# Kernel optimization log

Measured on AMD Instinct MI355X. Metric: run time of the kernel, lower is better.

The kernel has to match this reference:

```python
import jax, jax.numpy as jnp
import numpy as np

GRID_SIZE = 16
SPLINE_ORDER = 4
GRID_LO, GRID_HI = -1.0, 1.0
NUM_GRID = 2 * SPLINE_ORDER + GRID_SIZE + 1  # 25 knots
NUM_COEFFS = GRID_SIZE + SPLINE_ORDER        # 20 basis functions
B, IN_F, OUT_F = 2048, 512, 512


def _make_grid():
    h = (GRID_HI - GRID_LO) / GRID_SIZE
    t1 = -SPLINE_ORDER * h + GRID_LO
    t2 = (GRID_SIZE + SPLINE_ORDER + 1) * h + GRID_LO
    return jnp.linspace(t1, t2, NUM_GRID)


def _bspline_basis(x, grid):
    # x: [..., in]; returns [..., in, NUM_COEFFS] via De Boor recursion
    xe = x[..., None]
    bases = ((xe >= grid[:-1]) & (xe < grid[1:])).astype(x.dtype)
    for k in range(1, SPLINE_ORDER + 1):
        left = (xe - grid[:-k - 1]) / (grid[k:-1] - grid[:-k - 1]) * bases[..., :-1]
        right = (grid[k + 1:] - xe) / (grid[k + 1:] - grid[1:-k]) * bases[..., 1:]
        bases = left + right
    return bases


def setup_inputs() -> dict:
    key = jax.random.key(0)
    ks = jax.random.split(key, 5)
    fan = np.sqrt(1.0 / IN_F)
    return {
        "x": jax.random.normal(ks[0], (B, IN_F), jnp.float32),
        "prelu_weight": jax.random.normal(ks[1], (OUT_F, IN_F), jnp.float32) * 0.25,
        "base_weight": jax.random.uniform(ks[2], (OUT_F, IN_F), jnp.float32, -fan, fan),
        "spline_weight": jax.random.uniform(ks[3], (OUT_F, IN_F), jnp.float32, -fan, fan),
        "spline_coeffs": jax.random.normal(ks[4], (OUT_F, IN_F, NUM_COEFFS), jnp.float32) * 0.1,
    }


def reference(x, prelu_weight, base_weight, spline_weight, spline_coeffs):
    grid = _make_grid()
    xc = jnp.clip(x, GRID_LO, GRID_HI)
    pos = jax.nn.relu(xc)
    neg = xc - pos
    # base path: sum_j base_w[i,j]*(prelu_w[i,j]*neg[b,j] + pos[b,j])
    # fused: never materialize the [out, B, in] prelu output
    base = neg @ (base_weight * prelu_weight).T + pos @ base_weight.T  # [B, out]
    basis = _bspline_basis(xc, grid)  # [B, in, K]
    # spline path: fold spline_weight into coeffs, single contraction over (j,k)
    eff_coeffs = spline_weight[:, :, None] * spline_coeffs  # [out, in, K]
    spline = jnp.einsum('bjk,ijk->bi', basis, eff_coeffs)   # [B, out]
    return base + spline
```

## Files before the change

### kernel.cpp

```cpp
#include <hip/hip_runtime.h>


typedef _Float16 half_t;
typedef __attribute__((ext_vector_type(8))) _Float16 half8;
typedef __attribute__((ext_vector_type(4))) float floatx4;

#define B_DIM   2048
#define J_DIM   512
#define O_DIM   512
#define SLOTS   22
#define K_TOT   (J_DIM * SLOTS)
#define MTILE   128
#define NTILE   128
#define BK      32
#define KSPLIT  11
#define KS_LEN  (K_TOT / KSPLIT)
#define KCH     (KS_LEN / BK)
#define ZERO_BLKS 64

__device__ __forceinline__ void bspline5(float xc, int& k0, float Nv[5]) {
    const float invS = 7.68f;
    float u = (xc + 1.5f) * invS;
    int m = (int)u;
    m = min(max(m, 3), 19);
    k0 = m - 4;
    Nv[0] = 1.f; Nv[1] = 0.f; Nv[2] = 0.f; Nv[3] = 0.f; Nv[4] = 0.f;
#pragma unroll
    for (int d = 1; d <= 4; ++d) {
        float nw[5];
        float inv_d = 1.0f / (float)d;
#pragma unroll
        for (int r = 0; r < 5; ++r) {
            if (r > d) { nw[r] = 0.f; continue; }
            float kk = (float)(m - d + r);
            float acc = 0.f;
            if (r >= 1) acc += (u - kk) * Nv[r - 1];
            if (r < d)  acc += (kk + (float)(d + 1) - u) * Nv[r];
            nw[r] = acc * inv_d;
        }
#pragma unroll
        for (int r = 0; r < 5; ++r) Nv[r] = nw[r];
    }
}

__global__ __launch_bounds__(256) void prep_all(const float* __restrict__ x,
                                                const float* __restrict__ pw,
                                                const float* __restrict__ bw,
                                                const float* __restrict__ sw,
                                                const float* __restrict__ sc,
                                                half_t* __restrict__ A,
                                                half_t* __restrict__ Ct,
                                                float* __restrict__ out) {
    __shared__ half_t rec[J_DIM * SLOTS];
    int bid = blockIdx.x;
    int t = threadIdx.x;

    if (bid < ZERO_BLKS) {
        float4* o = (float4*)out;
        int base = bid * 4096;
#pragma unroll
        for (int i = 0; i < 16; ++i)
            o[base + i * 256 + t] = make_float4(0.f, 0.f, 0.f, 0.f);
        return;
    }

    if (bid < ZERO_BLKS + O_DIM) {
        int i = bid - ZERO_BLKS;
#pragma unroll
        for (int jj = 0; jj < 2; ++jj) {
            int j = t + jj * 256;
            size_t ij = (size_t)i * J_DIM + j;
            float s = sw[ij], b = bw[ij], p = pw[ij];
            const float4* scp4 = (const float4*)(sc + ij * 20);
            half_t* r = rec + j * SLOTS;
#pragma unroll
            for (int v = 0; v < 5; ++v) {
                float4 c4 = scp4[v];
                r[v * 4 + 0] = (half_t)(s * c4.x);
                r[v * 4 + 1] = (half_t)(s * c4.y);
                r[v * 4 + 2] = (half_t)(s * c4.z);
                r[v * 4 + 3] = (half_t)(s * c4.w);
            }
            r[20] = (half_t)(b * p);
            r[21] = (half_t)b;
        }
        __syncthreads();
        const uint4* src = (const uint4*)rec;
        uint4* dst = (uint4*)(Ct + (size_t)i * K_TOT);
        for (int idx = t; idx < (J_DIM * SLOTS * 2) / 16; idx += 256) dst[idx] = src[idx];
        return;
    }

    int b = bid - ZERO_BLKS - O_DIM;
#pragma unroll
    for (int jj = 0; jj < 2; ++jj) {
        int j = t + jj * 256;
        float xv = x[(size_t)b * J_DIM + j];
        float xc = fminf(fmaxf(xv, -1.f), 1.f);
        float pos = fmaxf(xc, 0.f);
        float neg = xc - pos;
        int k0; float Nv[5];
        bspline5(xc, k0, Nv);
        half_t* r = rec + j * SLOTS;
#pragma unroll
        for (int k = 0; k < 20; ++k) r[k] = (half_t)0.f;
#pragma unroll
        for (int rr = 0; rr < 5; ++rr) {
            int k = k0 + rr;
            if (k >= 0) r[k] = (half_t)Nv[rr];
        }
        r[20] = (half_t)neg;
        r[21] = (half_t)pos;
    }
    __syncthreads();
    const uint4* src = (const uint4*)rec;
    uint4* dst = (uint4*)(A + (size_t)b * K_TOT);
    for (int i = t; i < (J_DIM * SLOTS * 2) / 16; i += 256) dst[i] = src[i];
}

__global__ __launch_bounds__(256, 4) void gemm_f16(const half_t* __restrict__ A,
                                                   const half_t* __restrict__ Bt,
                                                   float* __restrict__ out) {
    __shared__ half_t As[2][MTILE * BK];
    __shared__ half_t Bs[2][NTILE * BK];

    int m0 = blockIdx.x * MTILE;
    int n0 = blockIdx.y * NTILE;
    int ks = blockIdx.z * KS_LEN;

    int t = threadIdx.x;
    int w = t >> 6;
    int l = t & 63;
    int wm = w >> 1, wn = w & 1;

    floatx4 acc[4][4] = {};

    int lrow = l >> 2;
    int lkof = (((l & 3) ^ ((l >> 3) & 3)) * 8);

    const half_t* gA = A + (size_t)m0 * K_TOT + ks;
    const half_t* gB = Bt + (size_t)n0 * K_TOT + ks;

    int q = l >> 4;
    int fr = l & 15;
    int qs = (q ^ ((fr >> 1) & 3)) * 8;

#define ISSUE_LOADS(c, p)                                                     \
    {                                                                         \
        int kb = (c) * BK;                                                    \
        _Pragma("unroll")                                                     \
        for (int n = 0; n < 2; ++n) {                                         \
            int r = (w * 2 + n) * 16 + lrow;                                  \
            __builtin_amdgcn_global_load_lds(                                 \
                (const __attribute__((address_space(1))) unsigned int*)       \
                    (gA + (size_t)r * K_TOT + kb + lkof),                     \
                (__attribute__((address_space(3))) unsigned int*)             \
                    (&As[p][0] + (w * 2 + n) * 512),                          \
                16, 0, 0);                                                    \
            __builtin_amdgcn_global_load_lds(                                 \
                (const __attribute__((address_space(1))) unsigned int*)       \
                    (gB + (size_t)r * K_TOT + kb + lkof),                     \
                (__attribute__((address_space(3))) unsigned int*)             \
                    (&Bs[p][0] + (w * 2 + n) * 512),                          \
                16, 0, 0);                                                    \
        }                                                                     \
    }

    ISSUE_LOADS(0, 0)
    int p = 0;
    for (int c = 0; c < KCH; ++c) {
        __syncthreads();
        if (c + 1 < KCH) ISSUE_LOADS(c + 1, p ^ 1)

        half8 af[4], bf[4];
#pragma unroll
        for (int mt = 0; mt < 4; ++mt)
            af[mt] = *(const half8*)(&As[p][0] + (wm * 64 + mt * 16 + fr) * BK + qs);
#pragma unroll
        for (int nt = 0; nt < 4; ++nt)
            bf[nt] = *(const half8*)(&Bs[p][0] + (wn * 64 + nt * 16 + fr) * BK + qs);
#pragma unroll
        for (int mt = 0; mt < 4; ++mt)
#pragma unroll
            for (int nt = 0; nt < 4; ++nt)
                acc[mt][nt] = __builtin_amdgcn_mfma_f32_16x16x32_f16(
                    af[mt], bf[nt], acc[mt][nt], 0, 0, 0);
        p ^= 1;
    }
#undef ISSUE_LOADS

#pragma unroll
    for (int mt = 0; mt < 4; ++mt)
#pragma unroll
        for (int nt = 0; nt < 4; ++nt) {
            int rr = m0 + wm * 64 + mt * 16 + q * 4;
            int cc = n0 + wn * 64 + nt * 16 + fr;
#pragma unroll
            for (int r = 0; r < 4; ++r)
                atomicAdd(out + (size_t)(rr + r) * O_DIM + cc, acc[mt][nt][r]);
        }
}

__global__ __launch_bounds__(256) void kan_fallback(const float* __restrict__ x,
                                                    const float* __restrict__ pw,
                                                    const float* __restrict__ bw,
                                                    const float* __restrict__ sw,
                                                    const float* __restrict__ sc,
                                                    float* __restrict__ out) {
    __shared__ float s_neg[J_DIM], s_pos[J_DIM], s_bas[J_DIM][5];
    __shared__ int s_k0[J_DIM];
    int b = blockIdx.x;
    int t = threadIdx.x;
#pragma unroll
    for (int jj = 0; jj < 2; ++jj) {
        int j = t + jj * 256;
        float xv = x[(size_t)b * J_DIM + j];
        float xc = fminf(fmaxf(xv, -1.f), 1.f);
        float pos = fmaxf(xc, 0.f);
        s_pos[j] = pos;
        s_neg[j] = xc - pos;
        int k0; float Nv[5];
        bspline5(xc, k0, Nv);
        s_k0[j] = k0;
#pragma unroll
        for (int r = 0; r < 5; ++r) s_bas[j][r] = Nv[r];
    }
    __syncthreads();
    for (int i = t; i < O_DIM; i += 256) {
        float acc = 0.f;
        for (int j = 0; j < J_DIM; ++j) {
            size_t ij = (size_t)i * J_DIM + j;
            float bwv = bw[ij];
            acc += bwv * (pw[ij] * s_neg[j] + s_pos[j]);
            int k0 = s_k0[j];
            const float* cp = sc + ij * 20;
            float sp = 0.f;
#pragma unroll
            for (int r = 0; r < 5; ++r) {
                int k = k0 + r;
                if (k >= 0) sp += s_bas[j][r] * cp[k];
            }
            acc += sw[ij] * sp;
        }
        out[(size_t)b * O_DIM + i] = acc;
    }
}

extern "C" void kernel_launch(void* const* d_in, const int* in_sizes, int n_in,
                              void* d_out, int out_size, void* d_ws, size_t ws_size,
                              hipStream_t stream) {
    const float* x  = (const float*)d_in[0];
    const float* pw = (const float*)d_in[1];
    const float* bw = (const float*)d_in[2];
    const float* sw = (const float*)d_in[3];
    const float* sc = (const float*)d_in[4];
    float* out = (float*)d_out;

    const size_t ws_needed = (size_t)(B_DIM + O_DIM) * K_TOT * sizeof(half_t);
    if (ws_size < ws_needed) {
        kan_fallback<<<B_DIM, 256, 0, stream>>>(x, pw, bw, sw, sc, out);
        return;
    }

    half_t* A  = (half_t*)d_ws;
    half_t* Ct = A + (size_t)B_DIM * K_TOT;

    prep_all<<<ZERO_BLKS + O_DIM + B_DIM, 256, 0, stream>>>(x, pw, bw, sw, sc, A, Ct, out);
    dim3 g(B_DIM / MTILE, O_DIM / NTILE, KSPLIT);
    gemm_f16<<<g, 256, 0, stream>>>(A, Ct, out);
}
```

Baseline: 142.5 us.

## Rewrite KAN pipeline with 256x256 split-K GEMM, partial buffers and reduce kernel

The GEMM moves from 128x128x32 tiles with atomicAdd split-K to 256x256x64 tiles with 512 threads, 16-way split-K and a block-index swizzle. Each K-split writes a private partial buffer, and a separate reduce kernel sums the partials, which removes float atomics and the output zeroing. Prep is rewritten to vectorize packing of weights and activations. The cost is extra workspace, a third launch and the traffic of 16 full partial outputs. Loads are staged with explicit vmcnt waits and setprio phases.

```diff
diff --git a/kernel.cpp b/kernel.cpp
--- a/kernel.cpp
+++ b/kernel.cpp
@@ -10,13 +10,10 @@
 #define O_DIM   512
 #define SLOTS   22
 #define K_TOT   (J_DIM * SLOTS)
-#define MTILE   128
-#define NTILE   128
-#define BK      32
-#define KSPLIT  11
-#define KS_LEN  (K_TOT / KSPLIT)
-#define KCH     (KS_LEN / BK)
-#define ZERO_BLKS 64
+#define BM      256
+#define BN      256
+#define BK      64
+#define KSPLIT  16
 
 __device__ __forceinline__ void bspline5(float xc, int& k0, float Nv[5]) {
     const float invS = 7.68f;
@@ -43,162 +40,224 @@
     }
 }
 
-__global__ __launch_bounds__(256) void prep_all(const float* __restrict__ x,
-                                                const float* __restrict__ pw,
-                                                const float* __restrict__ bw,
-                                                const float* __restrict__ sw,
-                                                const float* __restrict__ sc,
-                                                half_t* __restrict__ A,
-                                                half_t* __restrict__ Ct,
-                                                float* __restrict__ out) {
-    __shared__ half_t rec[J_DIM * SLOTS];
+__device__ __forceinline__ unsigned packh2(float a, float b) {
+    half_t ha = (half_t)a, hb = (half_t)b;
+    unsigned short ua = __builtin_bit_cast(unsigned short, ha);
+    unsigned short ub = __builtin_bit_cast(unsigned short, hb);
+    return (unsigned)ua | ((unsigned)ub << 16);
+}
+
+__global__ __launch_bounds__(256) void prep2(const float* __restrict__ x,
+                                             const float* __restrict__ pw,
+                                             const float* __restrict__ bw,
+                                             const float* __restrict__ sw,
+                                             const float* __restrict__ sc,
+                                             half_t* __restrict__ A,
+                                             half_t* __restrict__ Ct) {
+    __shared__ half_t sbuf[2][128 * 88];
     int bid = blockIdx.x;
     int t = threadIdx.x;
-
-    if (bid < ZERO_BLKS) {
-        float4* o = (float4*)out;
-        int base = bid * 4096;
-#pragma unroll
-        for (int i = 0; i < 16; ++i)
-            o[base + i * 256 + t] = make_float4(0.f, 0.f, 0.f, 0.f);
+    int sub = t >> 7;
+    int jq  = t & 127;
+    int j0  = jq * 4;
+
+    if (bid < 256) {
+        int i = bid * 2 + sub;
+        size_t ij0 = (size_t)i * J_DIM + j0;
+        float4 s4 = *(const float4*)(sw + ij0);
+        float4 b4 = *(const float4*)(bw + ij0);
+        float4 p4 = *(const float4*)(pw + ij0);
+        const float4* sp4 = (const float4*)(sc + ij0 * 20);
+        unsigned u[44];
+#pragma unroll
+        for (int jj = 0; jj < 4; ++jj) {
+            float s = ((const float*)&s4)[jj];
+            float b = ((const float*)&b4)[jj];
+            float p = ((const float*)&p4)[jj];
+#pragma unroll
+            for (int v = 0; v < 5; ++v) {
+                float4 c4 = sp4[jj * 5 + v];
+                u[jj * 11 + v * 2 + 0] = packh2(s * c4.x, s * c4.y);
+                u[jj * 11 + v * 2 + 1] = packh2(s * c4.z, s * c4.w);
+            }
+            u[jj * 11 + 10] = packh2(b * p, b);
+        }
+        uint4* dst = (uint4*)(Ct + (size_t)i * K_TOT + (size_t)j0 * SLOTS);
+#pragma unroll
+        for (int v = 0; v < 11; ++v)
+            dst[v] = make_uint4(u[4 * v], u[4 * v + 1], u[4 * v + 2], u[4 * v + 3]);
         return;
     }
 
-    if (bid < ZERO_BLKS + O_DIM) {
-        int i = bid - ZERO_BLKS;
-#pragma unroll
-        for (int jj = 0; jj < 2; ++jj) {
-            int j = t + jj * 256;
-            size_t ij = (size_t)i * J_DIM + j;
-            float s = sw[ij], b = bw[ij], p = pw[ij];
-            const float4* scp4 = (const float4*)(sc + ij * 20);
-            half_t* r = rec + j * SLOTS;
-#pragma unroll
-            for (int v = 0; v < 5; ++v) {
-                float4 c4 = scp4[v];
-                r[v * 4 + 0] = (half_t)(s * c4.x);
-                r[v * 4 + 1] = (half_t)(s * c4.y);
-                r[v * 4 + 2] = (half_t)(s * c4.z);
-                r[v * 4 + 3] = (half_t)(s * c4.w);
-            }
-            r[20] = (half_t)(b * p);
-            r[21] = (half_t)b;
-        }
-        __syncthreads();
-        const uint4* src = (const uint4*)rec;
-        uint4* dst = (uint4*)(Ct + (size_t)i * K_TOT);
-        for (int idx = t; idx < (J_DIM * SLOTS * 2) / 16; idx += 256) dst[idx] = src[idx];
-        return;
-    }
-
-    int b = bid - ZERO_BLKS - O_DIM;
-#pragma unroll
-    for (int jj = 0; jj < 2; ++jj) {
-        int j = t + jj * 256;
-        float xv = x[(size_t)b * J_DIM + j];
+    int b0 = (bid - 256) * 2;
+    int b = b0 + sub;
+    float4 x4 = *(const float4*)(x + (size_t)b * J_DIM + j0);
+    half_t* reg = &sbuf[sub][jq * 88];
+
+    half8 z;
+#pragma unroll
+    for (int e = 0; e < 8; ++e) z[e] = (half_t)0.f;
+#pragma unroll
+    for (int v = 0; v < 11; ++v) *(half8*)(reg + v * 8) = z;
+
+#pragma unroll
+    for (int jj = 0; jj < 4; ++jj) {
+        float xv = ((const float*)&x4)[jj];
         float xc = fminf(fmaxf(xv, -1.f), 1.f);
         float pos = fmaxf(xc, 0.f);
         float neg = xc - pos;
         int k0; float Nv[5];
         bspline5(xc, k0, Nv);
-        half_t* r = rec + j * SLOTS;
-#pragma unroll
-        for (int k = 0; k < 20; ++k) r[k] = (half_t)0.f;
+        half_t* rb = reg + jj * SLOTS;
 #pragma unroll
         for (int rr = 0; rr < 5; ++rr) {
             int k = k0 + rr;
-            if (k >= 0) r[k] = (half_t)Nv[rr];
-        }
-        r[20] = (half_t)neg;
-        r[21] = (half_t)pos;
+            if (k >= 0) rb[k] = (half_t)Nv[rr];
+        }
+        *(unsigned*)(rb + 20) = packh2(neg, pos);
     }
     __syncthreads();
-    const uint4* src = (const uint4*)rec;
-    uint4* dst = (uint4*)(A + (size_t)b * K_TOT);
-    for (int i = t; i < (J_DIM * SLOTS * 2) / 16; i += 256) dst[i] = src[i];
-}
-
-__global__ __launch_bounds__(256, 4) void gemm_f16(const half_t* __restrict__ A,
-                                                   const half_t* __restrict__ Bt,
-                                                   float* __restrict__ out) {
-    __shared__ half_t As[2][MTILE * BK];
-    __shared__ half_t Bs[2][NTILE * BK];
-
-    int m0 = blockIdx.x * MTILE;
-    int n0 = blockIdx.y * NTILE;
-    int ks = blockIdx.z * KS_LEN;
+
+    const uint4* src = (const uint4*)&sbuf[0][0];
+    uint4* dst = (uint4*)(A + (size_t)b0 * K_TOT);
+#pragma unroll
+    for (int v = 0; v < 11; ++v) dst[v * 256 + t] = src[v * 256 + t];
+}
+
+__global__ __launch_bounds__(512, 2) void gemm16_f16(const half_t* __restrict__ A,
+                                                     const half_t* __restrict__ Bt,
+                                                     float* __restrict__ out) {
+    constexpr int KS_LEN = K_TOT / KSPLIT;
+    constexpr int NSTEP = KS_LEN / BK;
+
+    __shared__ half_t As[2][BM * BK];
+    __shared__ half_t Bs[2][BN * BK];
+
+    int lid = blockIdx.x + 8 * (blockIdx.y + 2 * blockIdx.z);
+    int c = lid & 7;
+    int r = lid >> 3;
+    int bz = c + 8 * (r & 1);
+    int rr = r >> 1;
+    int bx = rr & 7;
+    int by = rr >> 3;
+
+    int m0 = bx * BM, n0 = by * BN, ks = bz * KS_LEN;
 
     int t = threadIdx.x;
-    int w = t >> 6;
-    int l = t & 63;
-    int wm = w >> 1, wn = w & 1;
-
-    floatx4 acc[4][4] = {};
-
-    int lrow = l >> 2;
-    int lkof = (((l & 3) ^ ((l >> 3) & 3)) * 8);
+    int w = t >> 6, l = t & 63;
+    int wm = w >> 2, wn = w & 3;
+    int q = l >> 4, fr = l & 15;
 
     const half_t* gA = A + (size_t)m0 * K_TOT + ks;
     const half_t* gB = Bt + (size_t)n0 * K_TOT + ks;
 
-    int q = l >> 4;
-    int fr = l & 15;
-    int qs = (q ^ ((fr >> 1) & 3)) * 8;
-
-#define ISSUE_LOADS(c, p)                                                     \
+    int srow = l >> 3;
+    int sq = ((l & 7) ^ srow) * 8;
+    int fsw0 = ((q)     ^ (fr & 7)) * 8;
+    int fsw1 = ((4 + q) ^ (fr & 7)) * 8;
+
+    floatx4 acc[8][4] = {};
+
+#define ISSUE(kb, p)                                                          \
     {                                                                         \
-        int kb = (c) * BK;                                                    \
         _Pragma("unroll")                                                     \
-        for (int n = 0; n < 2; ++n) {                                         \
-            int r = (w * 2 + n) * 16 + lrow;                                  \
+        for (int s = 0; s < 4; ++s)                                           \
             __builtin_amdgcn_global_load_lds(                                 \
                 (const __attribute__((address_space(1))) unsigned int*)       \
-                    (gA + (size_t)r * K_TOT + kb + lkof),                     \
+                    (gA + (size_t)(w * 32 + s * 8 + srow) * K_TOT + (kb) + sq),\
                 (__attribute__((address_space(3))) unsigned int*)             \
-                    (&As[p][0] + (w * 2 + n) * 512),                          \
+                    (&As[p][(w * 32 + s * 8) * BK]),                          \
                 16, 0, 0);                                                    \
+        _Pragma("unroll")                                                     \
+        for (int s = 0; s < 4; ++s)                                           \
             __builtin_amdgcn_global_load_lds(                                 \
                 (const __attribute__((address_space(1))) unsigned int*)       \
-                    (gB + (size_t)r * K_TOT + kb + lkof),                     \
+                    (gB + (size_t)(w * 32 + s * 8 + srow) * K_TOT + (kb) + sq),\
                 (__attribute__((address_space(3))) unsigned int*)             \
-                    (&Bs[p][0] + (w * 2 + n) * 512),                          \
+                    (&Bs[p][(w * 32 + s * 8) * BK]),                          \
                 16, 0, 0);                                                    \
+    }
+
+#define AFRD(mt, kss) (*(const half8*)(Ab + ((wm << 7) + ((mt) << 4) + fr) * BK + (kss)))
+#define BFRD(nt, kss) (*(const half8*)(Bb + ((wn << 6) + ((nt) << 4) + fr) * BK + (kss)))
+
+#define PHASE(p, EXTRA)                                                       \
+    {                                                                         \
+        half8 a0 = AFRD(2 * (p), fsw0), a1 = AFRD(2 * (p), fsw1);             \
+        half8 a2 = AFRD(2 * (p) + 1, fsw0), a3 = AFRD(2 * (p) + 1, fsw1);     \
+        EXTRA                                                                 \
+        __builtin_amdgcn_s_barrier();                                         \
+        __builtin_amdgcn_s_setprio(1);                                        \
+        _Pragma("unroll")                                                     \
+        for (int nt = 0; nt < 4; ++nt) {                                      \
+            acc[2 * (p)][nt] = __builtin_amdgcn_mfma_f32_16x16x32_f16(        \
+                a0, bfr[nt][0], acc[2 * (p)][nt], 0, 0, 0);                   \
+            acc[2 * (p)][nt] = __builtin_amdgcn_mfma_f32_16x16x32_f16(        \
+                a1, bfr[nt][1], acc[2 * (p)][nt], 0, 0, 0);                   \
+            acc[2 * (p) + 1][nt] = __builtin_amdgcn_mfma_f32_16x16x32_f16(    \
+                a2, bfr[nt][0], acc[2 * (p) + 1][nt], 0, 0, 0);               \
+            acc[2 * (p) + 1][nt] = __builtin_amdgcn_mfma_f32_16x16x32_f16(    \
+                a3, bfr[nt][1], acc[2 * (p) + 1][nt], 0, 0, 0);               \
         }                                                                     \
-    }
-
-    ISSUE_LOADS(0, 0)
-    int p = 0;
-    for (int c = 0; c < KCH; ++c) {
-        __syncthreads();
-        if (c + 1 < KCH) ISSUE_LOADS(c + 1, p ^ 1)
-
-        half8 af[4], bf[4];
-#pragma unroll
-        for (int mt = 0; mt < 4; ++mt)
-            af[mt] = *(const half8*)(&As[p][0] + (wm * 64 + mt * 16 + fr) * BK + qs);
-#pragma unroll
-        for (int nt = 0; nt < 4; ++nt)
-            bf[nt] = *(const half8*)(&Bs[p][0] + (wn * 64 + nt * 16 + fr) * BK + qs);
-#pragma unroll
-        for (int mt = 0; mt < 4; ++mt)
-#pragma unroll
-            for (int nt = 0; nt < 4; ++nt)
-                acc[mt][nt] = __builtin_amdgcn_mfma_f32_16x16x32_f16(
-                    af[mt], bf[nt], acc[mt][nt], 0, 0, 0);
-        p ^= 1;
-    }
-#undef ISSUE_LOADS
-
-#pragma unroll
-    for (int mt = 0; mt < 4; ++mt)
+        __builtin_amdgcn_s_setprio(0);                                        \
+        __builtin_amdgcn_s_barrier();                                         \
+    }
+
+    ISSUE(0, 0)
+    ISSUE(BK, 1)
+
+    for (int T = 0; T < NSTEP; ++T) {
+        if (T < NSTEP - 1) { asm volatile("s_waitcnt vmcnt(8)" ::: "memory"); }
+        else               { asm volatile("s_waitcnt vmcnt(0)" ::: "memory"); }
+        __builtin_amdgcn_s_barrier();
+
+        const half_t* Ab = &As[T & 1][0];
+        const half_t* Bb = &Bs[T & 1][0];
+        half8 bfr[4][2];
+
+        PHASE(0,
+            _Pragma("unroll")
+            for (int nt = 0; nt < 4; ++nt) {
+                bfr[nt][0] = BFRD(nt, fsw0);
+                bfr[nt][1] = BFRD(nt, fsw1);
+            }
+        )
+        PHASE(1, )
+        PHASE(2, )
+        PHASE(3, )
+
+        if (T + 2 < NSTEP) ISSUE((T + 2) * BK, T & 1)
+    }
+#undef PHASE
+#undef AFRD
+#undef BFRD
+#undef ISSUE
+
+    float* dst = out + (size_t)bz * ((size_t)B_DIM * O_DIM);
+#pragma unroll
+    for (int mt = 0; mt < 8; ++mt)
 #pragma unroll
         for (int nt = 0; nt < 4; ++nt) {
-            int rr = m0 + wm * 64 + mt * 16 + q * 4;
+            int rw = m0 + wm * 128 + mt * 16 + q * 4;
             int cc = n0 + wn * 64 + nt * 16 + fr;
 #pragma unroll
-            for (int r = 0; r < 4; ++r)
-                atomicAdd(out + (size_t)(rr + r) * O_DIM + cc, acc[mt][nt][r]);
-        }
+            for (int rg = 0; rg < 4; ++rg)
+                dst[(size_t)(rw + rg) * O_DIM + cc] = acc[mt][nt][rg];
+        }
+}
+
+__global__ __launch_bounds__(256) void reduce16(const float* __restrict__ parts,
+                                                float* __restrict__ out) {
+    constexpr int N4 = B_DIM * O_DIM / 4;
+    int i = blockIdx.x * 256 + threadIdx.x;
+    const float4* p = (const float4*)parts;
+    float4 a = p[i];
+#pragma unroll
+    for (int z = 1; z < KSPLIT; ++z) {
+        float4 b = p[(size_t)z * N4 + i];
+        a.x += b.x; a.y += b.y; a.z += b.z; a.w += b.w;
+    }
+    ((float4*)out)[i] = a;
 }
 
 __global__ __launch_bounds__(256) void kan_fallback(const float* __restrict__ x,
@@ -256,16 +315,19 @@
     const float* sc = (const float*)d_in[4];
     float* out = (float*)d_out;
 
-    const size_t ws_needed = (size_t)(B_DIM + O_DIM) * K_TOT * sizeof(half_t);
-    if (ws_size < ws_needed) {
+    const size_t abct = (size_t)(B_DIM + O_DIM) * K_TOT * sizeof(half_t);
+    const size_t parts_bytes = (size_t)KSPLIT * B_DIM * O_DIM * sizeof(float);
+
+    if (ws_size >= abct + parts_bytes) {
+        half_t* A  = (half_t*)d_ws;
+        half_t* Ct = A + (size_t)B_DIM * K_TOT;
+        float* parts = (float*)((char*)d_ws + abct);
+
+        prep2<<<256 + B_DIM / 2, 256, 0, stream>>>(x, pw, bw, sw, sc, A, Ct);
+        dim3 g(B_DIM / BM, O_DIM / BN, KSPLIT);
+        gemm16_f16<<<g, 512, 0, stream>>>(A, Ct, parts);
+        reduce16<<<(B_DIM * O_DIM / 4) / 256, 256, 0, stream>>>(parts, out);
+    } else {
         kan_fallback<<<B_DIM, 256, 0, stream>>>(x, pw, bw, sw, sc, out);
-        return;
-    }
-
-    half_t* A  = (half_t*)d_ws;
-    half_t* Ct = A + (size_t)B_DIM * K_TOT;
-
-    prep_all<<<ZERO_BLKS + O_DIM + B_DIM, 256, 0, stream>>>(x, pw, bw, sw, sc, A, Ct, out);
-    dim3 g(B_DIM / MTILE, O_DIM / NTILE, KSPLIT);
-    gemm_f16<<<g, 256, 0, stream>>>(A, Ct, out);
-}
+    }
+}
```

After: 137.2 us. 1.04x faster.
